# Performance work log

Hardware: AMD Instinct MI355X
Metric: run time of the kernel (lower is better)

## Reference

```python
import jax, jax.numpy as jnp
import numpy as np
import math

S_DIM = 512
Z_DIM = 64
B, L = 64, 512
NUM_HEADS = 4
HEAD_DIM = S_DIM // NUM_HEADS
N_AA = 20


def _layer_norm(x, eps=1e-5):
    mu = jnp.mean(x, axis=-1, keepdims=True)
    var = jnp.var(x, axis=-1, keepdims=True)
    return (x - mu) * jax.lax.rsqrt(var + eps)


def setup_inputs() -> dict:
    key = jax.random.key(0)
    ks = jax.random.split(key, 16)
    scale = 0.02
    d = {
        's': jax.random.normal(ks[0], (B, L, S_DIM), jnp.float32),
        'z': jax.random.normal(ks[1], (B, L, Z_DIM), jnp.float32),
        'wq': jax.random.normal(ks[2], (S_DIM, S_DIM), jnp.float32) * scale,
        'bq': jnp.zeros((S_DIM,), jnp.float32),
        'wk': jax.random.normal(ks[3], (S_DIM, S_DIM), jnp.float32) * scale,
        'bk': jnp.zeros((S_DIM,), jnp.float32),
        'wv': jax.random.normal(ks[4], (S_DIM, S_DIM), jnp.float32) * scale,
        'bv': jnp.zeros((S_DIM,), jnp.float32),
        'wo': jax.random.normal(ks[5], (S_DIM, S_DIM), jnp.float32) * scale,
        'bo': jnp.zeros((S_DIM,), jnp.float32),
        'wp': jax.random.normal(ks[6], (S_DIM, N_AA), jnp.float32) * scale,
        'bp': jnp.zeros((N_AA,), jnp.float32),
        'pos_bias': jax.random.normal(ks[7], (512,), jnp.float32) * 0.3,
        'entropy_weight': jnp.ones((1,), jnp.float32) * 0.1,
        'ln_g': jnp.ones((S_DIM,), jnp.float32),
        'ln_b': jnp.zeros((S_DIM,), jnp.float32),
        'w1': jax.random.normal(ks[8], (S_DIM, 4 * S_DIM), jnp.float32) * scale,
        'b1': jnp.zeros((4 * S_DIM,), jnp.float32),
        'w2': jax.random.normal(ks[9], (4 * S_DIM, S_DIM), jnp.float32) * scale,
        'b2': jnp.zeros((S_DIM,), jnp.float32),
    }
    return d


def reference(s, z, wq, bq, wk, bk, wv, bv, wo, bo, wp, bp, pos_bias,
              entropy_weight, ln_g, ln_b, w1, b1, w2, b2):
    Bc, Lc, D = s.shape
    H, hd = NUM_HEADS, D // NUM_HEADS

    s_ln = _layer_norm(s)  # non-affine F.layer_norm

    # sequence-profile entropy
    logits = s_ln @ wp + bp                      # [B,L,20]
    profile_probs = jax.nn.softmax(logits, axis=-1)
    position_entropy = -jnp.sum(profile_probs * jnp.log(profile_probs + 1e-8), axis=-1)  # [B,L]

    q = (s_ln @ wq + bq).reshape(Bc, Lc, H, hd)
    k = (s_ln @ wk + bk).reshape(Bc, Lc, H, hd)
    v = (s_ln @ wv + bv).reshape(Bc, Lc, H, hd)

    scores = jnp.einsum('blhd,bmhd->bhlm', q, k) / math.sqrt(hd)  # [B,H,L,L]

    # bias injected only at query index 0, using batch-0 entropy (as in torch code)
    entropy_guidance = -position_entropy[0, :Lc] * entropy_weight[0]  # [L]
    total_bias = entropy_guidance + pos_bias[:Lc]                      # [L]
    scores = scores.at[:, :, 0, :].add(total_bias[None, None, :])

    attn_weights = jax.nn.softmax(scores, axis=-1)                     # [B,H,L,L]
    attn_out = jnp.einsum('bhlm,bmhd->blhd', attn_weights, v).reshape(Bc, Lc, D)

    s2 = s + (attn_out @ wo + bo)

    h = _layer_norm(s2) * ln_g + ln_b
    ffn_out = jax.nn.relu(h @ w1 + b1) @ w2 + b2
    s3 = s2 + ffn_out

    return (s3, z, attn_weights[:, 0, :, :], position_entropy, profile_probs)
```

## Files before the change

### kernel.cpp

```cpp
#include <hip/hip_runtime.h>
#include <hip/hip_bf16.h>
#include <math.h>

#define SDIM 512
#define BATCH 64
#define LSEQ 512
#define NHEAD 4
#define HDIM 128
#define NAA 20
#define NROWS (BATCH * LSEQ)
#define LDQKV 1536

typedef __attribute__((ext_vector_type(8))) short short8;
typedef __attribute__((ext_vector_type(4))) float f32x4;

__device__ __forceinline__ unsigned short f2bf(float f) {
    unsigned int x = __float_as_uint(f);
    unsigned int r = (x + 0x7fffu + ((x >> 16) & 1u)) >> 16;
    return (unsigned short)r;
}
__device__ __forceinline__ float bf2f(unsigned short u) {
    return __uint_as_float((unsigned int)u << 16);
}

__device__ __forceinline__ void load16_lds(const void* g, void* lds) {
    __builtin_amdgcn_global_load_lds(
        (const __attribute__((address_space(1))) unsigned int*)g,
        (__attribute__((address_space(3))) unsigned int*)lds, 16, 0, 0);
}

__global__ __launch_bounds__(256) void wtrans(
    const float* __restrict__ W, unsigned short* __restrict__ Wt, int K, int N)
{
    __shared__ float tile[32][33];
    const int t = threadIdx.x, tx = t & 31, ty = t >> 5;
    const int n0 = blockIdx.x * 32, k0 = blockIdx.y * 32;
    #pragma unroll
    for (int p = 0; p < 4; p++)
        tile[ty + p * 8][tx] = W[(size_t)(k0 + ty + p * 8) * N + n0 + tx];
    __syncthreads();
    #pragma unroll
    for (int p = 0; p < 4; p++)
        Wt[(size_t)(n0 + ty + p * 8) * K + k0 + tx] = f2bf(tile[tx][ty + p * 8]);
}

__global__ __launch_bounds__(256) void wptrans(
    const float* __restrict__ wp, unsigned short* __restrict__ wpT)
{
    const int g = blockIdx.x * 256 + threadIdx.x;
    const int k = g & 511, j = g >> 9;
    float v = (j < NAA) ? wp[(size_t)k * NAA + j] : 0.0f;
    wpT[(size_t)j * 512 + k] = f2bf(v);
}

__global__ void bpack(const float* __restrict__ bq, const float* __restrict__ bk,
                      const float* __restrict__ bv, float* __restrict__ bqkv)
{
    int t = threadIdx.x;
    bqkv[t] = bq[t]; bqkv[512 + t] = bk[t]; bqkv[1024 + t] = bv[t];
}

template<int INMODE, bool AFFINE>
__global__ __launch_bounds__(256) void ln_kernel(
    const void* __restrict__ inp, unsigned short* __restrict__ out,
    const float* __restrict__ gamma, const float* __restrict__ beta)
{
    const int w = threadIdx.x >> 6, l = threadIdx.x & 63;
    const int r = blockIdx.x * 4 + w;

    float x[8];
    if (INMODE == 0) {
        const float* row = (const float*)inp + (size_t)r * SDIM;
        float4 a = *(const float4*)(row + l * 4);
        float4 b = *(const float4*)(row + 256 + l * 4);
        x[0] = a.x; x[1] = a.y; x[2] = a.z; x[3] = a.w;
        x[4] = b.x; x[5] = b.y; x[6] = b.z; x[7] = b.w;
    } else {
        const unsigned short* row = (const unsigned short*)inp + (size_t)r * SDIM;
        uint2 a = *(const uint2*)(row + l * 4);
        uint2 b = *(const uint2*)(row + 256 + l * 4);
        x[0] = bf2f((unsigned short)(a.x & 0xffff)); x[1] = bf2f((unsigned short)(a.x >> 16));
        x[2] = bf2f((unsigned short)(a.y & 0xffff)); x[3] = bf2f((unsigned short)(a.y >> 16));
        x[4] = bf2f((unsigned short)(b.x & 0xffff)); x[5] = bf2f((unsigned short)(b.x >> 16));
        x[6] = bf2f((unsigned short)(b.y & 0xffff)); x[7] = bf2f((unsigned short)(b.y >> 16));
    }

    float sum = 0.f, sq = 0.f;
    #pragma unroll
    for (int i = 0; i < 8; i++) { sum += x[i]; sq += x[i] * x[i]; }
    #pragma unroll
    for (int o = 1; o < 64; o <<= 1) {
        sum += __shfl_xor(sum, o);
        sq  += __shfl_xor(sq, o);
    }
    const float mean = sum * (1.0f / SDIM);
    const float var  = sq * (1.0f / SDIM) - mean * mean;
    const float inv  = rsqrtf(var + 1e-5f);

    float y[8];
    if (AFFINE) {
        float4 g0 = *(const float4*)(gamma + l * 4);
        float4 g1 = *(const float4*)(gamma + 256 + l * 4);
        float4 b0 = *(const float4*)(beta + l * 4);
        float4 b1 = *(const float4*)(beta + 256 + l * 4);
        y[0] = (x[0]-mean)*inv*g0.x + b0.x; y[1] = (x[1]-mean)*inv*g0.y + b0.y;
        y[2] = (x[2]-mean)*inv*g0.z + b0.z; y[3] = (x[3]-mean)*inv*g0.w + b0.w;
        y[4] = (x[4]-mean)*inv*g1.x + b1.x; y[5] = (x[5]-mean)*inv*g1.y + b1.y;
        y[6] = (x[6]-mean)*inv*g1.z + b1.z; y[7] = (x[7]-mean)*inv*g1.w + b1.w;
    } else {
        #pragma unroll
        for (int i = 0; i < 8; i++) y[i] = (x[i] - mean) * inv;
    }

    unsigned short* orow = out + (size_t)r * SDIM;
    uint2 p0, p1;
    p0.x = (unsigned)f2bf(y[0]) | ((unsigned)f2bf(y[1]) << 16);
    p0.y = (unsigned)f2bf(y[2]) | ((unsigned)f2bf(y[3]) << 16);
    p1.x = (unsigned)f2bf(y[4]) | ((unsigned)f2bf(y[5]) << 16);
    p1.y = (unsigned)f2bf(y[6]) | ((unsigned)f2bf(y[7]) << 16);
    *(uint2*)(orow + l * 4)       = p0;
    *(uint2*)(orow + 256 + l * 4) = p1;
}

__global__ __launch_bounds__(256) void profile_kernel(
    const unsigned short* __restrict__ A,
    const unsigned short* __restrict__ wpT,
    const float* __restrict__ bp,
    float* __restrict__ probs,
    float* __restrict__ pe)
{
    __shared__ __align__(16) unsigned short As[128 * 64];

    const int t = threadIdx.x;
    const int w = t >> 6, l = t & 63;
    const int lr = l & 15, lg = l >> 4;
    const int m0 = blockIdx.x * 128;

    f32x4 sacc[2][2];
    #pragma unroll
    for (int m = 0; m < 2; m++)
        #pragma unroll
        for (int n = 0; n < 2; n++)
            sacc[m][n] = (f32x4){0.f, 0.f, 0.f, 0.f};

    const int srow  = l >> 3;
    const int swz16 = ((l & 7) ^ srow) << 4;
    const char* pA[4];
    unsigned ldsoff[4];
    #pragma unroll
    for (int i = 0; i < 4; i++) {
        const int row = (w * 4 + i) * 8 + srow;
        pA[i] = (const char*)A + (size_t)(m0 + row) * 1024 + swz16;
        ldsoff[i] = (unsigned)(w * 4 + i) * 1024;
    }

    const int rsw   = (lr & 7) << 4;
    const int foff0 = (lg * 16) ^ rsw;
    const int foff1 = (64 + lg * 16) ^ rsw;
    int arow[2];
    #pragma unroll
    for (int m = 0; m < 2; m++) arow[m] = (w * 32 + m * 16 + lr) * 128;

    for (int k0 = 0; k0 < 512; k0 += 64) {
        const size_t kb = (size_t)k0 * 2;
        #pragma unroll
        for (int i = 0; i < 4; i++)
            load16_lds(pA[i] + kb, (char*)As + ldsoff[i]);
        __syncthreads();

        short8 af[2], bf[2];
        #pragma unroll
        for (int m = 0; m < 2; m++) af[m] = *(const short8*)((const char*)As + arow[m] + foff0);
        #pragma unroll
        for (int n = 0; n < 2; n++)
            bf[n] = *(const short8*)(wpT + (size_t)(n * 16 + lr) * 512 + k0 + lg * 8);
        #pragma unroll
        for (int m = 0; m < 2; m++)
            #pragma unroll
            for (int n = 0; n < 2; n++)
                sacc[m][n] = __builtin_amdgcn_mfma_f32_16x16x32_bf16(af[m], bf[n], sacc[m][n], 0, 0, 0);

        #pragma unroll
        for (int m = 0; m < 2; m++) af[m] = *(const short8*)((const char*)As + arow[m] + foff1);
        #pragma unroll
        for (int n = 0; n < 2; n++)
            bf[n] = *(const short8*)(wpT + (size_t)(n * 16 + lr) * 512 + k0 + 32 + lg * 8);
        #pragma unroll
        for (int m = 0; m < 2; m++)
            #pragma unroll
            for (int n = 0; n < 2; n++)
                sacc[m][n] = __builtin_amdgcn_mfma_f32_16x16x32_bf16(af[m], bf[n], sacc[m][n], 0, 0, 0);

        __syncthreads();
    }

    const float b0 = bp[lr];
    const float b1 = (lr < 4) ? bp[16 + lr] : 0.0f;
    #pragma unroll
    for (int m = 0; m < 2; m++) {
        #pragma unroll
        for (int j = 0; j < 4; j++) {
            const float v0 = sacc[m][0][j] + b0;
            const float e0 = __expf(v0);
            const float v1 = sacc[m][1][j] + b1;
            const float e1 = (lr < 4) ? __expf(v1) : 0.0f;
            float Sp = e0 + e1;
            float Tp = e0 * v0 + ((lr < 4) ? e1 * v1 : 0.0f);
            #pragma unroll
            for (int o = 1; o < 16; o <<= 1) {
                Sp += __shfl_xor(Sp, o);
                Tp += __shfl_xor(Tp, o);
            }
            const float inv = 1.0f / Sp;
            const int row = m0 + w * 32 + m * 16 + lg * 4 + j;
            probs[(size_t)row * NAA + lr] = e0 * inv;
            if (lr < 4) probs[(size_t)row * NAA + 16 + lr] = e1 * inv;
            if (lr == 0) pe[row] = logf(Sp) - Tp * inv;
        }
    }
}

__global__ void bias_kernel(const float* __restrict__ pe,
                            const float* __restrict__ ew,
                            const float* __restrict__ pos,
                            float* __restrict__ tb)
{
    int t = threadIdx.x;
    tb[t] = -pe[t] * ew[0] + pos[t];
}

template<int OMODE, bool BIAS, bool RELU, int RESID>
__global__ __launch_bounds__(256, 2) void mgemm3(
    const unsigned short* __restrict__ A, int lda,
    const unsigned short* __restrict__ Bt, int ldb,
    void* __restrict__ Cv, int ldc,
    const float* __restrict__ bias,
    const void* __restrict__ R, int ldr,
    int K)
{
    __shared__ __align__(16) char lds[65536];

    const int t = threadIdx.x;
    const int w = t >> 6, l = t & 63;
    const int wr = w >> 1, wc = w & 1;
    const int lg = l >> 4, lr = l & 15;

    const int gx   = gridDim.x;
    const int nwg  = gx * gridDim.y;
    const int flat = blockIdx.x + gx * blockIdx.y;
    const int cpx  = nwg >> 3;
    const int logical = (flat & 7) * cpx + (flat >> 3);
    const int m0 = (logical / gx) * 128, n0 = (logical % gx) * 128;

    f32x4 acc[4][4];
    #pragma unroll
    for (int m = 0; m < 4; m++)
        #pragma unroll
        for (int n = 0; n < 4; n++)
            acc[m][n] = (f32x4){0.f, 0.f, 0.f, 0.f};

    const char* srcA[2];
    const char* srcB[2];
    #pragma unroll
    for (int j = 0; j < 2; j++) {
        const int s   = j * 256 + t;
        const int r2  = s >> 3, cc = s & 7;
        const int ccs = cc ^ (r2 & 7);
        const int grow = r2 * 2 + (ccs >> 2);
        const int gch  = ccs & 3;
        srcA[j] = (const char*)A  + ((size_t)(m0 + grow) * lda + gch * 8) * 2;
        srcB[j] = (const char*)Bt + ((size_t)(n0 + grow) * ldb + gch * 8) * 2;
    }

    const int nt = K >> 5;

    auto stage = [&](int kt) {
        char* db = (char*)lds + (kt & 3) * 16384;
        const size_t kb = (size_t)kt * 64;
        #pragma unroll
        for (int j = 0; j < 2; j++) {
            load16_lds(srcA[j] + kb, db + j * 4096 + t * 16);
            load16_lds(srcB[j] + kb, db + 8192 + j * 4096 + t * 16);
        }
    };

    stage(0); stage(1); stage(2);

    const int laneoff = (lr >> 1) * 128 + (((((lr & 1) << 2) | lg) ^ (lr >> 1)) << 4);

    for (int kt = 0; kt < nt; ++kt) {
        const int rem = nt - 1 - kt;
        if (rem >= 2)      { asm volatile("s_waitcnt vmcnt(8)" ::: "memory"); }
        else if (rem == 1) { asm volatile("s_waitcnt vmcnt(4)" ::: "memory"); }
        else               { asm volatile("s_waitcnt vmcnt(0)" ::: "memory"); }
        __builtin_amdgcn_s_barrier();
        asm volatile("" ::: "memory");

        if (kt + 3 < nt) stage(kt + 3);

        const char* Ab = (const char*)lds + (kt & 3) * 16384;
        const char* Bb = Ab + 8192;

        short8 af[4], bf[4];
        #pragma unroll
        for (int m = 0; m < 4; m++)
            af[m] = *(const short8*)(Ab + wr * 4096 + m * 1024 + laneoff);
        #pragma unroll
        for (int n = 0; n < 4; n++)
            bf[n] = *(const short8*)(Bb + wc * 4096 + n * 1024 + laneoff);

        __builtin_amdgcn_s_setprio(1);
        #pragma unroll
        for (int m = 0; m < 4; m++)
            #pragma unroll
            for (int n = 0; n < 4; n++)
                acc[m][n] = __builtin_amdgcn_mfma_f32_16x16x32_bf16(af[m], bf[n], acc[m][n], 0, 0, 0);
        __builtin_amdgcn_s_setprio(0);
        asm volatile("" ::: "memory");
    }

    #pragma unroll
    for (int n = 0; n < 4; n++) {
        const int col = n0 + wc * 64 + n * 16 + lr;
        const float bv = BIAS ? bias[col] : 0.0f;
        #pragma unroll
        for (int m = 0; m < 4; m++) {
            const int rb = m0 + wr * 64 + m * 16 + lg * 4;
            #pragma unroll
            for (int j = 0; j < 4; j++) {
                float v = acc[m][n][j] + bv;
                if (RELU) v = fmaxf(v, 0.f);
                const size_t row = (size_t)(rb + j);
                if (RESID == 1) v += ((const float*)R)[row * ldr + col];
                if (RESID == 2) v += bf2f(((const unsigned short*)R)[row * ldr + col]);
                if (OMODE == 0) {
                    ((float*)Cv)[row * ldc + col] = v;
                } else {
                    ((unsigned short*)Cv)[row * ldc + col] = f2bf(v);
                }
            }
        }
    }
}

__global__ __launch_bounds__(256, 3) void attn_mfma(
    const unsigned short* __restrict__ QKV,
    const float* __restrict__ tb,
    unsigned short* __restrict__ AOb,
    float* __restrict__ lgout)
{
    const int flat = blockIdx.x + 4 * (blockIdx.y + 4 * blockIdx.z);
    const int logical = ((flat & 7) << 7) + (flat >> 3);
    const int qt = logical & 3;
    const int h  = (logical >> 2) & 3;
    const int b  = logical >> 4;
    const int t  = threadIdx.x;
    const int w  = t >> 6, l = t & 63;
    const int lr = l & 15, lg = l >> 4;
    const int qbase = qt * 128 + w * 32;

    const unsigned short* Qp = QKV;
    const unsigned short* Kp = QKV + 512;
    const unsigned short* Vp = QKV + 1024;

    __shared__ __align__(16) unsigned short Ks[64 * 128];
    __shared__ __align__(16) unsigned short Vt[128 * 64];
    __shared__ __align__(16) unsigned short Pl[4 * 2048];
    __shared__ float tbs[512];

    tbs[t] = tb[t];
    tbs[t + 256] = tb[t + 256];

    short8 qf[2][4];
    #pragma unroll
    for (int fc = 0; fc < 2; fc++) {
        const size_t qrow = (size_t)(b * LSEQ + qbase + fc * 16 + lr) * LDQKV + h * HDIM;
        #pragma unroll
        for (int ks = 0; ks < 4; ks++)
            qf[fc][ks] = *(const short8*)(Qp + qrow + ks * 32 + lg * 8);
    }

    f32x4 oacc[2][8];
    #pragma unroll
    for (int m = 0; m < 2; m++)
        #pragma unroll
        for (int n = 0; n < 8; n++)
            oacc[m][n] = (f32x4){0.f, 0.f, 0.f, 0.f};
    float lpart[2] = {0.f, 0.f};

    const float scale = 0.08838834764831845f;
    unsigned short* Plw = Pl + w * 2048;

    for (int kt = 0; kt < 8; ++kt) {
        __syncthreads();

        const int k0 = (l & 31) * 2;
        const int d0 = w * 32 + (l >> 5) * 16;
        const size_t vrow = (size_t)(b * LSEQ + kt * 64 + k0) * LDQKV + h * HDIM + d0;
        short8 va0 = *(const short8*)(Vp + vrow);
        short8 va1 = *(const short8*)(Vp + vrow + 8);
        short8 vb0 = *(const short8*)(Vp + vrow + LDQKV);
        short8 vb1 = *(const short8*)(Vp + vrow + LDQKV + 8);

        #pragma unroll
        for (int it = 0; it < 4; it++) {
            const int bi = it * 4 + w;
            const int r  = bi * 4 + lg;
            const int sc = lr ^ (r & 7);
            const char* src = (const char*)Kp +
                (size_t)(b * LSEQ + kt * 64 + r) * (LDQKV * 2) + h * 256 + sc * 16;
            load16_lds(src, (char*)Ks + bi * 1024);
        }

        #pragma unroll
        for (int j = 0; j < 16; j++) {
            const int d = d0 + j;
            unsigned short lo = (unsigned short)((j < 8) ? va0[j] : va1[j - 8]);
            unsigned short hi = (unsigned short)((j < 8) ? vb0[j] : vb1[j - 8]);
            unsigned int pk = (unsigned)lo | ((unsigned)hi << 16);
            const int addr = d * 128 + ((((k0 >> 3) ^ (d & 7))) << 4) + (k0 & 7) * 2;
            *(unsigned int*)((char*)Vt + addr) = pk;
        }
        __syncthreads();

        f32x4 sacc[4][2];
        #pragma unroll
        for (int fm = 0; fm < 4; fm++)
            #pragma unroll
            for (int fc = 0; fc < 2; fc++)
                sacc[fm][fc] = (f32x4){0.f, 0.f, 0.f, 0.f};
        #pragma unroll
        for (int ks = 0; ks < 4; ks++) {
            short8 af[4];
            #pragma unroll
            for (int fm = 0; fm < 4; fm++) {
                const int r2 = fm * 16 + lr;
                af[fm] = *(const short8*)((const char*)Ks +
                          r2 * 256 + (((ks * 4 + lg) ^ (lr & 7)) << 4));
            }
            #pragma unroll
            for (int fm = 0; fm < 4; fm++)
                #pragma unroll
                for (int fc = 0; fc < 2; fc++)
                    sacc[fm][fc] = __builtin_amdgcn_mfma_f32_16x16x32_bf16(
                        af[fm], qf[fc][ks], sacc[fm][fc], 0, 0, 0);
        }

        #pragma unroll
        for (int fm = 0; fm < 4; fm++) {
            #pragma unroll
            for (int fc = 0; fc < 2; fc++) {
                float p0 = sacc[fm][fc][0] * scale;
                float p1 = sacc[fm][fc][1] * scale;
                float p2 = sacc[fm][fc][2] * scale;
                float p3 = sacc[fm][fc][3] * scale;
                if (qt == 0 && w == 0 && fc == 0 && lr == 0) {
                    const int kb = kt * 64 + fm * 16 + lg * 4;
                    p0 += tbs[kb + 0]; p1 += tbs[kb + 1];
                    p2 += tbs[kb + 2]; p3 += tbs[kb + 3];
                }
                p0 = __expf(p0); p1 = __expf(p1);
                p2 = __expf(p2); p3 = __expf(p3);
                lpart[fc] += (p0 + p1) + (p2 + p3);
                const int rq = fc * 16 + lr;
                const int chunk = fm * 2 + (lg >> 1);
                const int addr = rq * 128 + ((chunk ^ (rq & 7)) << 4) + (lg & 1) * 8;
                unsigned int lo = (unsigned)f2bf(p0) | ((unsigned)f2bf(p1) << 16);
                unsigned int hi = (unsigned)f2bf(p2) | ((unsigned)f2bf(p3) << 16);
                *(uint2*)((char*)Plw + addr) = make_uint2(lo, hi);
            }
        }

        #pragma unroll
        for (int ks2 = 0; ks2 < 2; ks2++) {
            short8 pf[2];
            #pragma unroll
            for (int fm2 = 0; fm2 < 2; fm2++) {
                const int rq2 = fm2 * 16 + lr;
                pf[fm2] = *(const short8*)((const char*)Plw +
                           rq2 * 128 + (((ks2 * 4 + lg) ^ (rq2 & 7)) << 4));
            }
            #pragma unroll
            for (int fn = 0; fn < 8; fn++) {
                const int d = fn * 16 + lr;
                short8 vf = *(const short8*)((const char*)Vt +
                             d * 128 + (((ks2 * 4 + lg) ^ (d & 7)) << 4));
                #pragma unroll
                for (int fm2 = 0; fm2 < 2; fm2++)
                    oacc[fm2][fn] = __builtin_amdgcn_mfma_f32_16x16x32_bf16(
                        pf[fm2], vf, oacc[fm2][fn], 0, 0, 0);
            }
        }
    }

    float l0 = lpart[0], l1 = lpart[1];
    l0 += __shfl_xor(l0, 16); l0 += __shfl_xor(l0, 32);
    l1 += __shfl_xor(l1, 16); l1 += __shfl_xor(l1, 32);
    float* lw = (float*)Plw;
    if (lg == 0) { lw[lr] = l0; lw[16 + lr] = l1; }
    if (h == 0 && lg == 0) {
        lgout[b * LSEQ + qbase + lr]      = l0;
        lgout[b * LSEQ + qbase + 16 + lr] = l1;
    }
    __builtin_amdgcn_s_waitcnt(0);

    #pragma unroll
    for (int fm2 = 0; fm2 < 2; fm2++) {
        float linv[4];
        #pragma unroll
        for (int j = 0; j < 4; j++)
            linv[j] = 1.0f / lw[fm2 * 16 + lg * 4 + j];
        #pragma unroll
        for (int fn = 0; fn < 8; fn++) {
            const int d = fn * 16 + lr;
            #pragma unroll
            for (int j = 0; j < 4; j++) {
                const int q = qbase + fm2 * 16 + lg * 4 + j;
                AOb[(size_t)(b * LSEQ + q) * SDIM + h * HDIM + d] =
                    f2bf(oacc[fm2][fn][j] * linv[j]);
            }
        }
    }
}

__global__ __launch_bounds__(256) void sw0_kernel(
    const unsigned short* __restrict__ QKV,
    const float* __restrict__ tb,
    const float* __restrict__ lsum,
    float* __restrict__ W0)
{
    const int flat = blockIdx.x + 4 * blockIdx.y;
    const int logical = ((flat & 7) << 5) + (flat >> 3);
    const int qt = logical & 3;
    const int b  = logical >> 2;
    const int t  = threadIdx.x;
    const int w  = t >> 6, l = t & 63;
    const int lr = l & 15, lg = l >> 4;
    const int qbase = qt * 128 + w * 32;

    const unsigned short* Qp = QKV;
    const unsigned short* Kp = QKV + 512;

    __shared__ __align__(16) unsigned short Ks[64 * 128];

    short8 qf[2][4];
    #pragma unroll
    for (int fc = 0; fc < 2; fc++) {
        const size_t qrow = (size_t)(b * LSEQ + qbase + fc * 16 + lr) * LDQKV;
        #pragma unroll
        for (int ks = 0; ks < 4; ks++)
            qf[fc][ks] = *(const short8*)(Qp + qrow + ks * 32 + lg * 8);
    }

    float linv[2];
    linv[0] = 1.0f / lsum[b * LSEQ + qbase + lr];
    linv[1] = 1.0f / lsum[b * LSEQ + qbase + 16 + lr];

    const float scale = 0.08838834764831845f;

    for (int kt = 0; kt < 8; ++kt) {
        __syncthreads();
        #pragma unroll
        for (int it = 0; it < 4; it++) {
            const int bi = it * 4 + w;
            const int r  = bi * 4 + lg;
            const int sc = lr ^ (r & 7);
            const char* src = (const char*)Kp +
                (size_t)(b * LSEQ + kt * 64 + r) * (LDQKV * 2) + sc * 16;
            load16_lds(src, (char*)Ks + bi * 1024);
        }
        __syncthreads();

        f32x4 sacc[4][2];
        #pragma unroll
        for (int fm = 0; fm < 4; fm++)
            #pragma unroll
            for (int fc = 0; fc < 2; fc++)
                sacc[fm][fc] = (f32x4){0.f, 0.f, 0.f, 0.f};
        #pragma unroll
        for (int ks = 0; ks < 4; ks++) {
            short8 af[4];
            #pragma unroll
            for (int fm = 0; fm < 4; fm++) {
                const int r2 = fm * 16 + lr;
                af[fm] = *(const short8*)((const char*)Ks +
                          r2 * 256 + (((ks * 4 + lg) ^ (lr & 7)) << 4));
            }
            #pragma unroll
            for (int fm = 0; fm < 4; fm++)
                #pragma unroll
                for (int fc = 0; fc < 2; fc++)
                    sacc[fm][fc] = __builtin_amdgcn_mfma_f32_16x16x32_bf16(
                        af[fm], qf[fc][ks], sacc[fm][fc], 0, 0, 0);
        }

        #pragma unroll
        for (int fm = 0; fm < 4; fm++) {
            #pragma unroll
            for (int fc = 0; fc < 2; fc++) {
                float p0 = sacc[fm][fc][0] * scale;
                float p1 = sacc[fm][fc][1] * scale;
                float p2 = sacc[fm][fc][2] * scale;
                float p3 = sacc[fm][fc][3] * scale;
                if (qt == 0 && w == 0 && fc == 0 && lr == 0) {
                    const int kb = kt * 64 + fm * 16 + lg * 4;
                    p0 += tb[kb + 0]; p1 += tb[kb + 1];
                    p2 += tb[kb + 2]; p3 += tb[kb + 3];
                }
                p0 = __expf(p0) * linv[fc]; p1 = __expf(p1) * linv[fc];
                p2 = __expf(p2) * linv[fc]; p3 = __expf(p3) * linv[fc];
                const int q = qbase + fc * 16 + lr;
                float* dst = W0 + (size_t)(b * LSEQ + q) * LSEQ +
                             kt * 64 + fm * 16 + lg * 4;
                *(float4*)dst = make_float4(p0, p1, p2, p3);
            }
        }
    }
}

extern "C" void kernel_launch(void* const* d_in, const int* in_sizes, int n_in,
                              void* d_out, int out_size, void* d_ws, size_t ws_size,
                              hipStream_t stream)
{
    const float* s   = (const float*)d_in[0];
    const float* z   = (const float*)d_in[1];
    const float* wq  = (const float*)d_in[2];
    const float* bq  = (const float*)d_in[3];
    const float* wk  = (const float*)d_in[4];
    const float* bk  = (const float*)d_in[5];
    const float* wv  = (const float*)d_in[6];
    const float* bv  = (const float*)d_in[7];
    const float* wo  = (const float*)d_in[8];
    const float* bo  = (const float*)d_in[9];
    const float* wp  = (const float*)d_in[10];
    const float* bp  = (const float*)d_in[11];
    const float* pos = (const float*)d_in[12];
    const float* ew  = (const float*)d_in[13];
    const float* lng = (const float*)d_in[14];
    const float* lnb = (const float*)d_in[15];
    const float* w1  = (const float*)d_in[16];
    const float* b1  = (const float*)d_in[17];
    const float* w2  = (const float*)d_in[18];
    const float* b2  = (const float*)d_in[19];

    float* out = (float*)d_out;
    const size_t oz  = (size_t)NROWS * SDIM;
    const size_t ow  = oz + (size_t)NROWS * 64;
    const size_t ope = ow + (size_t)NROWS * LSEQ;
    const size_t opr = ope + (size_t)NROWS;

    char* wsb = (char*)d_ws;
    unsigned short* QKV = (unsigned short*)(wsb);
    unsigned short* F   = (unsigned short*)(wsb);
    unsigned short* Xb  = (unsigned short*)(wsb + 100663296);
    unsigned short* s2b = (unsigned short*)(wsb + 134217728);
    unsigned short* hb  = (unsigned short*)(wsb + 167772160);
    unsigned short* wqkvt = (unsigned short*)(wsb + 234881024);
    unsigned short* wot = wqkvt + 786432;
    unsigned short* w1t = wqkvt + 1048576;
    unsigned short* w2t = wqkvt + 2097152;
    unsigned short* wpT = wqkvt + 3145728;
    float* bqkv = (float*)(wsb + 234881024 + 6324224);
    float* tb   = bqkv + 1536;
    float* lgv  = tb + 512;

    wtrans<<<dim3(16, 16), 256, 0, stream>>>(wq, wqkvt, 512, 512);
    wtrans<<<dim3(16, 16), 256, 0, stream>>>(wk, wqkvt + 262144, 512, 512);
    wtrans<<<dim3(16, 16), 256, 0, stream>>>(wv, wqkvt + 524288, 512, 512);
    wtrans<<<dim3(16, 16), 256, 0, stream>>>(wo, wot, 512, 512);
    wtrans<<<dim3(64, 16), 256, 0, stream>>>(w1, w1t, 512, 2048);
    wtrans<<<dim3(16, 64), 256, 0, stream>>>(w2, w2t, 2048, 512);
    wptrans<<<64, 256, 0, stream>>>(wp, wpT);
    bpack<<<1, 512, 0, stream>>>(bq, bk, bv, bqkv);

    ln_kernel<0, false><<<NROWS / 4, 256, 0, stream>>>(s, Xb, nullptr, nullptr);

    profile_kernel<<<256, 256, 0, stream>>>(Xb, wpT, bp, out + opr, out + ope);

    bias_kernel<<<1, 512, 0, stream>>>(out + ope, ew, pos, tb);

    mgemm3<1, true, false, 0><<<dim3(12, 256), 256, 0, stream>>>(
        Xb, 512, wqkvt, 512, QKV, LDQKV, bqkv, nullptr, 0, 512);

    attn_mfma<<<dim3(4, NHEAD, BATCH), 256, 0, stream>>>(
        QKV, tb, Xb, lgv);

    sw0_kernel<<<dim3(4, BATCH), 256, 0, stream>>>(QKV, tb, lgv, out + ow);

    mgemm3<1, true, false, 1><<<dim3(4, 256), 256, 0, stream>>>(
        Xb, 512, wot, 512, s2b, 512, bo, s, 512, 512);

    ln_kernel<1, true><<<NROWS / 4, 256, 0, stream>>>(s2b, hb, lng, lnb);

    mgemm3<1, true, true, 0><<<dim3(16, 256), 256, 0, stream>>>(
        hb, 512, w1t, 512, F, 2048, b1, nullptr, 0, 512);

    mgemm3<0, true, false, 2><<<dim3(4, 256), 256, 0, stream>>>(
        F, 2048, w2t, 2048, out, 512, b2, s2b, 512, 2048);

    hipMemcpyAsync(out + oz, z, (size_t)NROWS * 64 * sizeof(float),
                   hipMemcpyDeviceToDevice, stream);
}
```

Measured before the change: 488.9 us.

## Use three-stage GEMM pipeline for higher occupancy and stage attention-weight stores through LDS

The GEMM kernel drops from a 4-buffer to a 3-buffer LDS ring (48KB) and raises launch bounds to 3 workgroups per CU. This trades prefetch depth for more resident waves to hide latency. Separately, the attention-weight output kernel now writes its probability tile into a per-wave padded LDS scratch and reads it back so each row is stored as a contiguous 256-byte segment, instead of scattered 16-byte stores. That improves global write coalescing at the cost of extra LDS traffic and shared memory.

After: 484.3 us. About the same (-0.9%).

```diff
diff --git a/kernel.cpp b/kernel.cpp
--- a/kernel.cpp
+++ b/kernel.cpp
@@ -230,7 +230,7 @@
 }
 
 template<int OMODE, bool BIAS, bool RELU, int RESID>
-__global__ __launch_bounds__(256, 2) void mgemm3(
+__global__ __launch_bounds__(256, 3) void mgemm3(
     const unsigned short* __restrict__ A, int lda,
     const unsigned short* __restrict__ Bt, int ldb,
     void* __restrict__ Cv, int ldc,
@@ -238,7 +238,7 @@
     const void* __restrict__ R, int ldr,
     int K)
 {
-    __shared__ __align__(16) char lds[65536];
+    __shared__ __align__(16) char lds[49152];
 
     const int t = threadIdx.x;
     const int w = t >> 6, l = t & 63;
@@ -274,8 +274,8 @@
 
     const int nt = K >> 5;
 
-    auto stage = [&](int kt) {
-        char* db = (char*)lds + (kt & 3) * 16384;
+    auto stage = [&](int kt, int bb) {
+        char* db = (char*)lds + bb;
         const size_t kb = (size_t)kt * 64;
         #pragma unroll
         for (int j = 0; j < 2; j++) {
@@ -284,21 +284,22 @@
         }
     };
 
-    stage(0); stage(1); stage(2);
+    stage(0, 0);
+    stage(1, 16384);
+
+    int b0 = 0, b1 = 16384, b2 = 32768;
 
     const int laneoff = (lr >> 1) * 128 + (((((lr & 1) << 2) | lg) ^ (lr >> 1)) << 4);
 
     for (int kt = 0; kt < nt; ++kt) {
-        const int rem = nt - 1 - kt;
-        if (rem >= 2)      { asm volatile("s_waitcnt vmcnt(8)" ::: "memory"); }
-        else if (rem == 1) { asm volatile("s_waitcnt vmcnt(4)" ::: "memory"); }
-        else               { asm volatile("s_waitcnt vmcnt(0)" ::: "memory"); }
+        if (kt + 1 < nt) { asm volatile("s_waitcnt vmcnt(4)" ::: "memory"); }
+        else             { asm volatile("s_waitcnt vmcnt(0)" ::: "memory"); }
         __builtin_amdgcn_s_barrier();
         asm volatile("" ::: "memory");
 
-        if (kt + 3 < nt) stage(kt + 3);
-
-        const char* Ab = (const char*)lds + (kt & 3) * 16384;
+        if (kt + 2 < nt) stage(kt + 2, b2);
+
+        const char* Ab = (const char*)lds + b0;
         const char* Bb = Ab + 8192;
 
         short8 af[4], bf[4];
@@ -317,6 +318,8 @@
                 acc[m][n] = __builtin_amdgcn_mfma_f32_16x16x32_bf16(af[m], bf[n], acc[m][n], 0, 0, 0);
         __builtin_amdgcn_s_setprio(0);
         asm volatile("" ::: "memory");
+
+        const int tmp = b0; b0 = b1; b1 = b2; b2 = tmp;
     }
 
     #pragma unroll
@@ -542,6 +545,7 @@
     const unsigned short* Kp = QKV + 512;
 
     __shared__ __align__(16) unsigned short Ks[64 * 128];
+    __shared__ __align__(16) float Sc[4][32][68];
 
     short8 qf[2][4];
     #pragma unroll
@@ -609,11 +613,17 @@
                 }
                 p0 = __expf(p0) * linv[fc]; p1 = __expf(p1) * linv[fc];
                 p2 = __expf(p2) * linv[fc]; p3 = __expf(p3) * linv[fc];
-                const int q = qbase + fc * 16 + lr;
-                float* dst = W0 + (size_t)(b * LSEQ + q) * LSEQ +
-                             kt * 64 + fm * 16 + lg * 4;
-                *(float4*)dst = make_float4(p0, p1, p2, p3);
-            }
+                *(float4*)&Sc[w][fc * 16 + lr][fm * 16 + lg * 4] =
+                    make_float4(p0, p1, p2, p3);
+            }
+        }
+
+        #pragma unroll
+        for (int i = 0; i < 8; i++) {
+            const int row = i * 4 + lg;
+            float4 v = *(const float4*)&Sc[w][row][lr * 4];
+            *(float4*)(W0 + (size_t)(b * LSEQ + qbase + row) * LSEQ +
+                       kt * 64 + lr * 4) = v;
         }
     }
 }
```
